# Performance work log

Hardware: AMD Instinct MI355X
Metric: run time of the kernel (lower is better)

## Reference

```python
import jax, jax.numpy as jnp
from jax import lax
import numpy as np

DIM = 128    # block channel dim C
RESO = 56    # H = W = patches_resolution
HEADS = 4    # block num_heads (each branch uses HEADS//2)
SPLIT = 2    # split_size (stripe width)
MLP_RATIO = 4
BATCH = 32


def _ln(x, g, b, eps=1e-5):
    mu = jnp.mean(x, axis=-1, keepdims=True)
    var = jnp.mean(jnp.square(x - mu), axis=-1, keepdims=True)
    return (x - mu) * lax.rsqrt(var + eps) * g + b


def _lepe_attn(q, k, v, cw, cb, H, W, H_sp, W_sp, heads):
    # q,k,v: (B, L=H*W, C). Cross-shaped window attention with depthwise-conv LePE.
    B, L, C = q.shape
    hd = C // heads
    scale = hd ** -0.5
    nH, nW = H // H_sp, W // W_sp
    tok = H_sp * W_sp

    def to_win(t):  # im2cswin: (B,L,C) -> (B*nH*nW, heads, tok, hd)
        t = t.transpose(0, 2, 1).reshape(B, C, H, W)
        t = t.reshape(B, C, nH, H_sp, nW, W_sp).transpose(0, 2, 4, 3, 5, 1)
        return t.reshape(-1, tok, heads, hd).transpose(0, 2, 1, 3)

    qw = to_win(q) * scale
    kw = to_win(k)

    # v as per-window images (B*nW_total, C, H_sp, W_sp) for the depthwise conv LePE
    vimg = v.transpose(0, 2, 1).reshape(B, C, H, W)
    vimg = vimg.reshape(B, C, nH, H_sp, nW, W_sp).transpose(0, 2, 4, 1, 3, 5).reshape(-1, C, H_sp, W_sp)
    lepe = lax.conv_general_dilated(vimg, cw, (1, 1), 'SAME', feature_group_count=C,
                                    dimension_numbers=('NCHW', 'OIHW', 'NCHW')) + cb[None, :, None, None]
    lepe = lepe.reshape(-1, heads, hd, tok).transpose(0, 1, 3, 2)  # (W', heads, tok, hd)
    vw = vimg.reshape(-1, heads, hd, tok).transpose(0, 1, 3, 2)

    attn = jax.nn.softmax(jnp.einsum('whqd,whkd->whqk', qw, kw), axis=-1)
    out = jnp.einsum('whqk,whkd->whqd', attn, vw) + lepe        # (W', heads, tok, hd)
    out = out.transpose(0, 2, 1, 3).reshape(-1, tok, C)
    # windows2img -> (B, H*W, C)
    out = out.reshape(B, nH, nW, H_sp, W_sp, C).transpose(0, 1, 3, 2, 4, 5).reshape(B, H * W, C)
    return out


def setup_inputs() -> dict:
    key = jax.random.key(0)
    ks = jax.random.split(key, 12)
    B, L, C = BATCH, RESO * RESO, DIM
    Ch = C // 2
    Hid = C * MLP_RATIO
    s = 0.02
    f32 = jnp.float32
    return {
        'x':       jax.random.normal(ks[0], (B, L, C), f32),
        'norm1_g': jnp.ones((C,), f32), 'norm1_b': jnp.zeros((C,), f32),
        'qkv_w':   jax.random.normal(ks[1], (C, 3 * C), f32) * s,
        'proj_w':  jax.random.normal(ks[2], (C, C), f32) * s,
        'proj_b':  jnp.zeros((C,), f32),
        'conv_w0': jax.random.normal(ks[3], (Ch, 1, 3, 3), f32) * s,
        'conv_b0': jnp.zeros((Ch,), f32),
        'conv_w1': jax.random.normal(ks[4], (Ch, 1, 3, 3), f32) * s,
        'conv_b1': jnp.zeros((Ch,), f32),
        'norm2_g': jnp.ones((C,), f32), 'norm2_b': jnp.zeros((C,), f32),
        'fc1_w':   jax.random.normal(ks[5], (C, Hid), f32) * s,
        'fc1_b':   jnp.zeros((Hid,), f32),
        'fc2_w':   jax.random.normal(ks[6], (Hid, C), f32) * s,
        'fc2_b':   jnp.zeros((C,), f32),
    }


def reference(x, norm1_g, norm1_b, qkv_w, proj_w, proj_b, conv_w0, conv_b0,
              conv_w1, conv_b1, norm2_g, norm2_b, fc1_w, fc1_b, fc2_w, fc2_b):
    B, L, C = x.shape
    H = W = RESO
    Ch = C // 2
    h = HEADS // 2

    img = _ln(x, norm1_g, norm1_b)
    qkv = (img @ qkv_w).reshape(B, L, 3, C)
    q, k, v = qkv[:, :, 0], qkv[:, :, 1], qkv[:, :, 2]

    # branch 0 (idx=0): H_sp = reso, W_sp = split  |  branch 1 (idx=1): H_sp = split, W_sp = reso
    x1 = _lepe_attn(q[..., :Ch], k[..., :Ch], v[..., :Ch], conv_w0, conv_b0, H, W, H, SPLIT, h)
    x2 = _lepe_attn(q[..., Ch:], k[..., Ch:], v[..., Ch:], conv_w1, conv_b1, H, W, SPLIT, W, h)

    att = jnp.concatenate([x1, x2], axis=2) @ proj_w + proj_b
    x = x + att
    y = _ln(x, norm2_g, norm2_b)
    y = jax.nn.gelu(y @ fc1_w + fc1_b, approximate=False) @ fc2_w + fc2_b
    return x + y
```

## Files before the change

### kernel.cpp

```cpp
#include <hip/hip_runtime.h>
#include <hip/hip_bf16.h>
#include <math.h>

#define NTOK 100352
typedef __attribute__((ext_vector_type(8))) short short8_t;
typedef __attribute__((ext_vector_type(4))) float f32x4;

union I4S8 { int4 i; short h[8]; short8_t v; };

__device__ __forceinline__ short f2bf(float f) {
    union { float f; unsigned u; } x; x.f = f;
    unsigned r = x.u + 0x7FFFu + ((x.u >> 16) & 1u);
    return (short)(r >> 16);
}
__device__ __forceinline__ float bf2f(short s) {
    union { unsigned u; float f; } x; x.u = ((unsigned)(unsigned short)s) << 16;
    return x.f;
}

__global__ void prep_weights(const float* __restrict__ qkv_w, const float* __restrict__ proj_w,
                             const float* __restrict__ fc1_w, const float* __restrict__ fc2_w,
                             short* __restrict__ wt) {
    int idx = blockIdx.x * 256 + threadIdx.x;
    const float* src; int K, N, base;
    if (idx < 49152)       { src = qkv_w;  K = 128; N = 384; base = 0; }
    else if (idx < 65536)  { src = proj_w; K = 128; N = 128; base = 49152; }
    else if (idx < 131072) { src = fc1_w;  K = 128; N = 512; base = 65536; }
    else                   { src = fc2_w;  K = 512; N = 128; base = 131072; }
    int local = idx - base;
    int n = local / K, k = local - n * K;
    wt[idx] = f2bf(src[k * N + n]);
}

__global__ __launch_bounds__(256) void ln_kernel(const float* __restrict__ in,
                                                 const float* __restrict__ g,
                                                 const float* __restrict__ b,
                                                 short* __restrict__ out) {
    int token = blockIdx.x * 4 + (threadIdx.x >> 6);
    int lane = threadIdx.x & 63;
    const float2 v = *reinterpret_cast<const float2*>(in + (size_t)token * 128 + lane * 2);
    float s = v.x + v.y;
    float sq = v.x * v.x + v.y * v.y;
    #pragma unroll
    for (int m = 32; m >= 1; m >>= 1) {
        s  += __shfl_xor(s, m);
        sq += __shfl_xor(sq, m);
    }
    float mean = s * (1.0f / 128.0f);
    float var = sq * (1.0f / 128.0f) - mean * mean;
    float rstd = rsqrtf(var + 1e-5f);
    float2 gg = *reinterpret_cast<const float2*>(g + lane * 2);
    float2 bb = *reinterpret_cast<const float2*>(b + lane * 2);
    float o0 = (v.x - mean) * rstd * gg.x + bb.x;
    float o1 = (v.y - mean) * rstd * gg.y + bb.y;
    unsigned pack = ((unsigned)(unsigned short)f2bf(o0)) |
                    (((unsigned)(unsigned short)f2bf(o1)) << 16);
    *reinterpret_cast<unsigned*>(out + (size_t)token * 128 + lane * 2) = pack;
}

template<int EPI>
__global__ __launch_bounds__(256) void gemm_kernel(const short* __restrict__ A,
                                                   const short* __restrict__ BT,
                                                   const float* __restrict__ bias,
                                                   const float* __restrict__ res,
                                                   void* __restrict__ out,
                                                   int N, int K) {
    __shared__ short As[64][136];
    __shared__ short Bs[64][136];
    const int m0 = blockIdx.x * 64;
    const int n0 = blockIdx.y * 64;
    const int tid = threadIdx.x;
    const int w = tid >> 6, lane = tid & 63;
    const int r = lane & 15, g = lane >> 4;

    f32x4 acc[4] = { {0.f,0.f,0.f,0.f}, {0.f,0.f,0.f,0.f},
                     {0.f,0.f,0.f,0.f}, {0.f,0.f,0.f,0.f} };

    for (int kc = 0; kc < K; kc += 128) {
        for (int i = tid; i < 1024; i += 256) {
            int row = i >> 4, seg = i & 15;
            int4 va = *reinterpret_cast<const int4*>(A + (size_t)(m0 + row) * K + kc + seg * 8);
            *reinterpret_cast<int4*>(&As[row][seg * 8]) = va;
            int4 vb = *reinterpret_cast<const int4*>(BT + (size_t)(n0 + row) * K + kc + seg * 8);
            *reinterpret_cast<int4*>(&Bs[row][seg * 8]) = vb;
        }
        __syncthreads();
        #pragma unroll
        for (int ks = 0; ks < 4; ++ks) {
            short8_t af = *reinterpret_cast<const short8_t*>(&As[w * 16 + r][ks * 32 + g * 8]);
            #pragma unroll
            for (int nt = 0; nt < 4; ++nt) {
                short8_t bfr = *reinterpret_cast<const short8_t*>(&Bs[nt * 16 + r][ks * 32 + g * 8]);
                acc[nt] = __builtin_amdgcn_mfma_f32_16x16x32_bf16(af, bfr, acc[nt], 0, 0, 0);
            }
        }
        __syncthreads();
    }

    #pragma unroll
    for (int nt = 0; nt < 4; ++nt) {
        int col = n0 + nt * 16 + r;
        float bv = (EPI != 0) ? bias[col] : 0.f;
        #pragma unroll
        for (int j = 0; j < 4; ++j) {
            int row = m0 + w * 16 + g * 4 + j;
            float v = acc[nt][j];
            if (EPI == 0) {
                ((short*)out)[(size_t)row * N + col] = f2bf(v);
            } else if (EPI == 1) {
                ((float*)out)[(size_t)row * N + col] = v + bv + res[(size_t)row * N + col];
            } else {
                float t = v + bv;
                float ge = 0.5f * t * (1.0f + erff(t * 0.70710678118654752f));
                ((short*)out)[(size_t)row * N + col] = f2bf(ge);
            }
        }
    }
}

__global__ __launch_bounds__(256) void attn_kernel(const short* __restrict__ qkv,
                                                   const float* __restrict__ cw0,
                                                   const float* __restrict__ cb0,
                                                   const float* __restrict__ cw1,
                                                   const float* __restrict__ cb1,
                                                   short* __restrict__ attout) {
    __shared__ short P[112][120];
    __shared__ short vT[32][120];

    const int win = blockIdx.x;
    const int head = blockIdx.y;
    const int type = blockIdx.z;
    const int b = win / 28;
    const int wdx = win - b * 28;
    const int tid = threadIdx.x;
    const int wv = tid >> 6, lane = tid & 63;
    const int r = lane & 15, g = lane >> 4;
    const int chb = type * 64 + head * 32;
    const float* cw = type ? cw1 : cw0;
    const float* cb = type ? cb1 : cb0;

    auto rowof = [&](int t) -> int {
        int l;
        if (type == 0) { int hs = t >> 1, wsp = t & 1; l = hs * 56 + wdx * 2 + wsp; }
        else           { int hs = (t >= 56) ? 1 : 0, wsp = t - hs * 56; l = (wdx * 2 + hs) * 56 + wsp; }
        return b * 3136 + l;
    };

    for (int i = tid; i < 448; i += 256) {
        int tt = i >> 2, seg = i & 3;
        int roww = rowof(tt);
        I4S8 u; u.i = *reinterpret_cast<const int4*>(qkv + (size_t)roww * 384 + 256 + chb + seg * 8);
        #pragma unroll
        for (int j = 0; j < 8; ++j) vT[seg * 8 + j][tt] = u.h[j];
    }

    short8_t kf[7];
    #pragma unroll
    for (int nt = 0; nt < 7; ++nt) {
        int roww = rowof(nt * 16 + r);
        kf[nt] = *reinterpret_cast<const short8_t*>(qkv + (size_t)roww * 384 + 128 + chb + g * 8);
    }

    f32x4 sa[2][7];
    #pragma unroll
    for (int t = 0; t < 2; ++t)
        #pragma unroll
        for (int nt = 0; nt < 7; ++nt)
            sa[t][nt] = (f32x4){0.f, 0.f, 0.f, 0.f};

    #pragma unroll
    for (int t = 0; t < 2; ++t) {
        int mt = wv + 4 * t;
        if (mt < 7) {
            int roww = rowof(mt * 16 + r);
            short8_t af = *reinterpret_cast<const short8_t*>(qkv + (size_t)roww * 384 + chb + g * 8);
            #pragma unroll
            for (int nt = 0; nt < 7; ++nt)
                sa[t][nt] = __builtin_amdgcn_mfma_f32_16x16x32_bf16(af, kf[nt], sa[t][nt], 0, 0, 0);
        }
    }

    const float scale = 0.17677669529663687f;
    #pragma unroll
    for (int t = 0; t < 2; ++t) {
        int mt = wv + 4 * t;
        if (mt < 7) {
            #pragma unroll
            for (int j = 0; j < 4; ++j) {
                float sv[7];
                float mx = -1e30f;
                #pragma unroll
                for (int nt = 0; nt < 7; ++nt) { sv[nt] = sa[t][nt][j] * scale; mx = fmaxf(mx, sv[nt]); }
                #pragma unroll
                for (int m = 8; m >= 1; m >>= 1) mx = fmaxf(mx, __shfl_xor(mx, m));
                float sum = 0.f;
                #pragma unroll
                for (int nt = 0; nt < 7; ++nt) { sv[nt] = __expf(sv[nt] - mx); sum += sv[nt]; }
                #pragma unroll
                for (int m = 8; m >= 1; m >>= 1) sum += __shfl_xor(sum, m);
                float inv = 1.0f / sum;
                int row = mt * 16 + g * 4 + j;
                #pragma unroll
                for (int nt = 0; nt < 7; ++nt)
                    P[row][nt * 16 + r] = f2bf(sv[nt] * inv);
            }
        }
    }
    __syncthreads();

    #pragma unroll
    for (int t = 0; t < 4; ++t) {
        int idx = wv + 4 * t;
        if (idx < 14) {
            int mt = idx >> 1, nt = idx & 1;
            int m0 = mt * 16, n0 = nt * 16;
            f32x4 acc = {0.f, 0.f, 0.f, 0.f};
            #pragma unroll
            for (int ks = 0; ks < 4; ++ks) {
                short8_t pa, vb;
                if (ks < 3 || g < 2) {
                    int k0 = ks * 32 + g * 8;
                    pa = *reinterpret_cast<const short8_t*>(&P[m0 + r][k0]);
                    vb = *reinterpret_cast<const short8_t*>(&vT[n0 + r][k0]);
                } else {
                    #pragma unroll
                    for (int j = 0; j < 8; ++j) { pa[j] = 0; vb[j] = 0; }
                }
                acc = __builtin_amdgcn_mfma_f32_16x16x32_bf16(pa, vb, acc, 0, 0, 0);
            }
            int d = n0 + r;
            int cl = head * 32 + d;
            float w9[9];
            #pragma unroll
            for (int j = 0; j < 9; ++j) w9[j] = cw[cl * 9 + j];
            float cbias = cb[cl];
            #pragma unroll
            for (int j = 0; j < 4; ++j) {
                int tok = m0 + g * 4 + j;
                float v = acc[j];
                int hs, wsp;
                if (type == 0) { hs = tok >> 1; wsp = tok & 1; }
                else           { hs = (tok >= 56) ? 1 : 0; wsp = tok - hs * 56; }
                float lp = cbias;
                #pragma unroll
                for (int ky = 0; ky < 3; ++ky) {
                    int hh = hs + ky - 1;
                    bool okh = (type == 0) ? (hh >= 0 && hh < 56) : (hh >= 0 && hh < 2);
                    #pragma unroll
                    for (int kx = 0; kx < 3; ++kx) {
                        int wwp = wsp + kx - 1;
                        bool okw = (type == 0) ? (wwp >= 0 && wwp < 2) : (wwp >= 0 && wwp < 56);
                        if (okh && okw) {
                            int tt = (type == 0) ? (hh * 2 + wwp) : (hh * 56 + wwp);
                            lp += w9[ky * 3 + kx] * bf2f(vT[d][tt]);
                        }
                    }
                }
                v += lp;
                int roww = rowof(tok);
                attout[(size_t)roww * 128 + chb + d] = f2bf(v);
            }
        }
    }
}

extern "C" void kernel_launch(void* const* d_in, const int* in_sizes, int n_in,
                              void* d_out, int out_size, void* d_ws, size_t ws_size,
                              hipStream_t stream) {
    const float* x      = (const float*)d_in[0];
    const float* n1g    = (const float*)d_in[1];
    const float* n1b    = (const float*)d_in[2];
    const float* qkv_w  = (const float*)d_in[3];
    const float* proj_w = (const float*)d_in[4];
    const float* proj_b = (const float*)d_in[5];
    const float* cw0    = (const float*)d_in[6];
    const float* cb0    = (const float*)d_in[7];
    const float* cw1    = (const float*)d_in[8];
    const float* cb1    = (const float*)d_in[9];
    const float* n2g    = (const float*)d_in[10];
    const float* n2b    = (const float*)d_in[11];
    const float* fc1_w  = (const float*)d_in[12];
    const float* fc1_b  = (const float*)d_in[13];
    const float* fc2_w  = (const float*)d_in[14];
    const float* fc2_b  = (const float*)d_in[15];
    float* out = (float*)d_out;
    char* ws = (char*)d_ws;

    short* img   = (short*)(ws + 0);
    short* qkv   = (short*)(ws + 25690112);
    short* att   = (short*)(ws + 102760448);
    float* xres  = (float*)(ws + 128450560);
    short* wT    = (short*)(ws + 179830784);
    short* wqkvT  = wT;
    short* wprojT = wT + 49152;
    short* wfc1T  = wT + 65536;
    short* wfc2T  = wT + 131072;
    short* hidden = qkv;
    short* y2     = img;

    prep_weights<<<768, 256, 0, stream>>>(qkv_w, proj_w, fc1_w, fc2_w, wT);
    ln_kernel<<<25088, 256, 0, stream>>>(x, n1g, n1b, img);
    gemm_kernel<0><<<dim3(1568, 6), 256, 0, stream>>>(img, wqkvT, nullptr, nullptr, qkv, 384, 128);
    attn_kernel<<<dim3(896, 2, 2), 256, 0, stream>>>(qkv, cw0, cb0, cw1, cb1, att);
    gemm_kernel<1><<<dim3(1568, 2), 256, 0, stream>>>(att, wprojT, proj_b, x, xres, 128, 128);
    ln_kernel<<<25088, 256, 0, stream>>>(xres, n2g, n2b, y2);
    gemm_kernel<2><<<dim3(1568, 8), 256, 0, stream>>>(y2, wfc1T, fc1_b, nullptr, hidden, 512, 128);
    gemm_kernel<1><<<dim3(1568, 2), 256, 0, stream>>>(hidden, wfc2T, fc2_b, xres, out, 128, 512);
}
```

Before: 383.6 us.

## Use 128x128 GEMM tiles with direct global-to-LDS A loads and register B fragments

The GEMM kernel moves from 64x64 tiles to 128x128 tiles arranged as 2x2 waves, each computing a 64x64 sub-tile. A tiles are loaded straight from global memory into LDS with an XOR swizzle to avoid bank conflicts. B fragments are read from global memory directly into registers instead of being staged in shared memory. This cuts global re-reads of A and weights and raises MFMA work per load, at the cost of more accumulator registers (64 floats per thread), possibly lower occupancy, and uncoalesced B fragment loads.

```diff
diff --git a/kernel.cpp b/kernel.cpp
--- a/kernel.cpp
+++ b/kernel.cpp
@@ -17,6 +17,10 @@
     union { unsigned u; float f; } x; x.u = ((unsigned)(unsigned short)s) << 16;
     return x.f;
 }
+
+#define GLDS16(gsrc, ldst) __builtin_amdgcn_global_load_lds( \
+    (const __attribute__((address_space(1))) unsigned int*)(gsrc), \
+    (__attribute__((address_space(3))) unsigned int*)(ldst), 16, 0, 0)
 
 __global__ void prep_weights(const float* __restrict__ qkv_w, const float* __restrict__ proj_w,
                              const float* __restrict__ fc1_w, const float* __restrict__ fc2_w,
@@ -65,54 +69,75 @@
                                                    const float* __restrict__ res,
                                                    void* __restrict__ out,
                                                    int N, int K) {
-    __shared__ short As[64][136];
-    __shared__ short Bs[64][136];
-    const int m0 = blockIdx.x * 64;
-    const int n0 = blockIdx.y * 64;
+    __shared__ short As[128 * 64];
+    const int m0 = blockIdx.x * 128;
+    const int n0 = blockIdx.y * 128;
     const int tid = threadIdx.x;
     const int w = tid >> 6, lane = tid & 63;
+    const int wr = w >> 1, wc = w & 1;
     const int r = lane & 15, g = lane >> 4;
 
-    f32x4 acc[4] = { {0.f,0.f,0.f,0.f}, {0.f,0.f,0.f,0.f},
-                     {0.f,0.f,0.f,0.f}, {0.f,0.f,0.f,0.f} };
-
-    for (int kc = 0; kc < K; kc += 128) {
-        for (int i = tid; i < 1024; i += 256) {
-            int row = i >> 4, seg = i & 15;
-            int4 va = *reinterpret_cast<const int4*>(A + (size_t)(m0 + row) * K + kc + seg * 8);
-            *reinterpret_cast<int4*>(&As[row][seg * 8]) = va;
-            int4 vb = *reinterpret_cast<const int4*>(BT + (size_t)(n0 + row) * K + kc + seg * 8);
-            *reinterpret_cast<int4*>(&Bs[row][seg * 8]) = vb;
-        }
+    f32x4 acc[4][4];
+    #pragma unroll
+    for (int i = 0; i < 4; ++i)
+        #pragma unroll
+        for (int j = 0; j < 4; ++j) acc[i][j] = (f32x4){0.f, 0.f, 0.f, 0.f};
+
+    const int srow_in_issue = lane >> 3;
+    const int sseg_lane = lane & 7;
+
+    for (int kc = 0; kc < K; kc += 64) {
+        #pragma unroll
+        for (int t = 0; t < 4; ++t) {
+            int row = w * 32 + t * 8 + srow_in_issue;
+            int sseg = sseg_lane ^ (row & 7);
+            const short* gsrc = A + (size_t)(m0 + row) * K + kc + sseg * 8;
+            GLDS16(gsrc, &As[(w * 32 + t * 8) * 64]);
+        }
+        short8_t bfr[2][4];
+        #pragma unroll
+        for (int ks = 0; ks < 2; ++ks)
+            #pragma unroll
+            for (int nf = 0; nf < 4; ++nf) {
+                int brow = n0 + wc * 64 + nf * 16 + r;
+                bfr[ks][nf] = *reinterpret_cast<const short8_t*>(
+                    BT + (size_t)brow * K + kc + ks * 32 + g * 8);
+            }
         __syncthreads();
         #pragma unroll
-        for (int ks = 0; ks < 4; ++ks) {
-            short8_t af = *reinterpret_cast<const short8_t*>(&As[w * 16 + r][ks * 32 + g * 8]);
-            #pragma unroll
-            for (int nt = 0; nt < 4; ++nt) {
-                short8_t bfr = *reinterpret_cast<const short8_t*>(&Bs[nt * 16 + r][ks * 32 + g * 8]);
-                acc[nt] = __builtin_amdgcn_mfma_f32_16x16x32_bf16(af, bfr, acc[nt], 0, 0, 0);
+        for (int ks = 0; ks < 2; ++ks) {
+            #pragma unroll
+            for (int mf = 0; mf < 4; ++mf) {
+                int arow = wr * 64 + mf * 16 + r;
+                int s0 = (ks * 4 + g) ^ (arow & 7);
+                short8_t af = *reinterpret_cast<const short8_t*>(&As[arow * 64 + s0 * 8]);
+                #pragma unroll
+                for (int nf = 0; nf < 4; ++nf)
+                    acc[mf][nf] = __builtin_amdgcn_mfma_f32_16x16x32_bf16(af, bfr[ks][nf], acc[mf][nf], 0, 0, 0);
             }
         }
         __syncthreads();
     }
 
     #pragma unroll
-    for (int nt = 0; nt < 4; ++nt) {
-        int col = n0 + nt * 16 + r;
+    for (int nf = 0; nf < 4; ++nf) {
+        int col = n0 + wc * 64 + nf * 16 + r;
         float bv = (EPI != 0) ? bias[col] : 0.f;
         #pragma unroll
-        for (int j = 0; j < 4; ++j) {
-            int row = m0 + w * 16 + g * 4 + j;
-            float v = acc[nt][j];
-            if (EPI == 0) {
-                ((short*)out)[(size_t)row * N + col] = f2bf(v);
-            } else if (EPI == 1) {
-                ((float*)out)[(size_t)row * N + col] = v + bv + res[(size_t)row * N + col];
-            } else {
-                float t = v + bv;
-                float ge = 0.5f * t * (1.0f + erff(t * 0.70710678118654752f));
-                ((short*)out)[(size_t)row * N + col] = f2bf(ge);
+        for (int mf = 0; mf < 4; ++mf) {
+            #pragma unroll
+            for (int j = 0; j < 4; ++j) {
+                int row = m0 + wr * 64 + mf * 16 + g * 4 + j;
+                float v = acc[mf][nf][j];
+                if (EPI == 0) {
+                    ((short*)out)[(size_t)row * N + col] = f2bf(v);
+                } else if (EPI == 1) {
+                    ((float*)out)[(size_t)row * N + col] = v + bv + res[(size_t)row * N + col];
+                } else {
+                    float t = v + bv;
+                    float ge = 0.5f * t * (1.0f + erff(t * 0.70710678118654752f));
+                    ((short*)out)[(size_t)row * N + col] = f2bf(ge);
+                }
             }
         }
     }
@@ -300,10 +325,10 @@
 
     prep_weights<<<768, 256, 0, stream>>>(qkv_w, proj_w, fc1_w, fc2_w, wT);
     ln_kernel<<<25088, 256, 0, stream>>>(x, n1g, n1b, img);
-    gemm_kernel<0><<<dim3(1568, 6), 256, 0, stream>>>(img, wqkvT, nullptr, nullptr, qkv, 384, 128);
+    gemm_kernel<0><<<dim3(784, 3), 256, 0, stream>>>(img, wqkvT, nullptr, nullptr, qkv, 384, 128);
     attn_kernel<<<dim3(896, 2, 2), 256, 0, stream>>>(qkv, cw0, cb0, cw1, cb1, att);
-    gemm_kernel<1><<<dim3(1568, 2), 256, 0, stream>>>(att, wprojT, proj_b, x, xres, 128, 128);
+    gemm_kernel<1><<<dim3(784, 1), 256, 0, stream>>>(att, wprojT, proj_b, x, xres, 128, 128);
     ln_kernel<<<25088, 256, 0, stream>>>(xres, n2g, n2b, y2);
-    gemm_kernel<2><<<dim3(1568, 8), 256, 0, stream>>>(y2, wfc1T, fc1_b, nullptr, hidden, 512, 128);
-    gemm_kernel<1><<<dim3(1568, 2), 256, 0, stream>>>(hidden, wfc2T, fc2_b, xres, out, 128, 512);
-}
+    gemm_kernel<2><<<dim3(784, 4), 256, 0, stream>>>(y2, wfc1T, fc1_b, nullptr, hidden, 512, 128);
+    gemm_kernel<1><<<dim3(784, 1), 256, 0, stream>>>(hidden, wfc2T, fc2_b, xres, out, 128, 512);
+}
```

After: 401.1 us. 1.05x slower.

## Fuse MLP fc1+GELU+fc2 via LDS and use register-resident weight GEMMs

Applied to the files above, without the earlier changes.

Replaces the LDS-staged GEMM with a kernel that keeps the 64-column weight slice in registers and streams A fragments directly from global memory, with several M tiles per block and vectorised packed stores. Fuses fc1, GELU and fc2 into one kernel that holds the 512-wide hidden activation per 64-row tile in swizzled shared memory, so the large hidden tensor never goes to HBM. Replaces erff with a polynomial erf approximation (Abramowitz-Stegun) for GELU. The risks are slightly less accurate GELU, and register pressure and occupancy limits from the launch bounds.

```diff
diff --git a/kernel.cpp b/kernel.cpp
--- a/kernel.cpp
+++ b/kernel.cpp
@@ -16,6 +16,19 @@
 __device__ __forceinline__ float bf2f(short s) {
     union { unsigned u; float f; } x; x.u = ((unsigned)(unsigned short)s) << 16;
     return x.f;
+}
+__device__ __forceinline__ unsigned pk2(float a, float b) {
+    return ((unsigned)(unsigned short)f2bf(a)) | (((unsigned)(unsigned short)f2bf(b)) << 16);
+}
+__device__ __forceinline__ float gelu(float x) {
+    float z = x * 0.70710678118654752f;
+    float az = fabsf(z);
+    float t = 1.0f / (1.0f + 0.3275911f * az);
+    float poly = t * (0.254829592f + t * (-0.284496736f + t * (1.421413741f +
+                 t * (-1.453152027f + t * 1.061405429f))));
+    float e = 1.0f - poly * __expf(-az * az);
+    float erfv = (z < 0.f) ? -e : e;
+    return 0.5f * x * (1.0f + erfv);
 }
 
 __global__ void prep_weights(const float* __restrict__ qkv_w, const float* __restrict__ proj_w,
@@ -58,62 +71,160 @@
     *reinterpret_cast<unsigned*>(out + (size_t)token * 128 + lane * 2) = pack;
 }
 
-template<int EPI>
-__global__ __launch_bounds__(256) void gemm_kernel(const short* __restrict__ A,
-                                                   const short* __restrict__ BT,
-                                                   const float* __restrict__ bias,
-                                                   const float* __restrict__ res,
-                                                   void* __restrict__ out,
-                                                   int N, int K) {
-    __shared__ short As[64][136];
-    __shared__ short Bs[64][136];
-    const int m0 = blockIdx.x * 64;
-    const int n0 = blockIdx.y * 64;
+template<int EPI, int IT>
+__global__ __launch_bounds__(256, 4) void sgemm(const short* __restrict__ A,
+                                                const short* __restrict__ WT,
+                                                const float* __restrict__ bias,
+                                                const float* __restrict__ resid,
+                                                short* __restrict__ outb,
+                                                float* __restrict__ outf,
+                                                int N) {
     const int tid = threadIdx.x;
     const int w = tid >> 6, lane = tid & 63;
     const int r = lane & 15, g = lane >> 4;
-
-    f32x4 acc[4] = { {0.f,0.f,0.f,0.f}, {0.f,0.f,0.f,0.f},
-                     {0.f,0.f,0.f,0.f}, {0.f,0.f,0.f,0.f} };
-
-    for (int kc = 0; kc < K; kc += 128) {
-        for (int i = tid; i < 1024; i += 256) {
-            int row = i >> 4, seg = i & 15;
-            int4 va = *reinterpret_cast<const int4*>(A + (size_t)(m0 + row) * K + kc + seg * 8);
-            *reinterpret_cast<int4*>(&As[row][seg * 8]) = va;
-            int4 vb = *reinterpret_cast<const int4*>(BT + (size_t)(n0 + row) * K + kc + seg * 8);
-            *reinterpret_cast<int4*>(&Bs[row][seg * 8]) = vb;
+    const int c0 = blockIdx.y * 64;
+    const int m0 = blockIdx.x * (64 * IT);
+
+    short8_t bfr[4][4];
+    #pragma unroll
+    for (int nt = 0; nt < 4; ++nt)
+        #pragma unroll
+        for (int kf = 0; kf < 4; ++kf)
+            bfr[nt][kf] = *reinterpret_cast<const short8_t*>(
+                WT + (size_t)(c0 + nt * 16 + r) * 128 + kf * 32 + g * 8);
+
+    #pragma unroll 2
+    for (int it = 0; it < IT; ++it) {
+        const int mrow = m0 + (it * 4 + w) * 16;
+        short8_t af[4];
+        #pragma unroll
+        for (int kf = 0; kf < 4; ++kf)
+            af[kf] = *reinterpret_cast<const short8_t*>(
+                A + (size_t)(mrow + r) * 128 + kf * 32 + g * 8);
+        f32x4 acc[4];
+        #pragma unroll
+        for (int nt = 0; nt < 4; ++nt) acc[nt] = (f32x4){0.f, 0.f, 0.f, 0.f};
+        #pragma unroll
+        for (int kf = 0; kf < 4; ++kf)
+            #pragma unroll
+            for (int nt = 0; nt < 4; ++nt)
+                acc[nt] = __builtin_amdgcn_mfma_f32_16x16x32_bf16(bfr[nt][kf], af[kf], acc[nt], 0, 0, 0);
+
+        const int row = mrow + r;
+        if (EPI == 0) {
+            #pragma unroll
+            for (int nt = 0; nt < 4; ++nt) {
+                int col = c0 + nt * 16 + g * 4;
+                uint2 p;
+                p.x = pk2(acc[nt][0], acc[nt][1]);
+                p.y = pk2(acc[nt][2], acc[nt][3]);
+                *reinterpret_cast<uint2*>(&outb[(size_t)row * N + col]) = p;
+            }
+        } else {
+            #pragma unroll
+            for (int nt = 0; nt < 4; ++nt) {
+                int col = c0 + nt * 16 + g * 4;
+                f32x4 b4 = *reinterpret_cast<const f32x4*>(&bias[col]);
+                f32x4 x4 = *reinterpret_cast<const f32x4*>(&resid[(size_t)row * 128 + col]);
+                f32x4 v;
+                #pragma unroll
+                for (int j = 0; j < 4; ++j) v[j] = acc[nt][j] + b4[j] + x4[j];
+                *reinterpret_cast<f32x4*>(&outf[(size_t)row * 128 + col]) = v;
+            }
+        }
+    }
+}
+
+__global__ __launch_bounds__(256, 4) void mlp_kernel(const short* __restrict__ Y,
+                                                     const short* __restrict__ W1T,
+                                                     const float* __restrict__ b1,
+                                                     const short* __restrict__ W2T,
+                                                     const float* __restrict__ b2,
+                                                     const float* __restrict__ xres,
+                                                     float* __restrict__ out) {
+    __shared__ short hid[64 * 256];
+    const int m0 = blockIdx.x * 64;
+    const int tid = threadIdx.x;
+    const int w = tid >> 6, lane = tid & 63;
+    const int r = lane & 15, g = lane >> 4;
+
+    f32x4 acc2[4][2];
+    #pragma unroll
+    for (int tt = 0; tt < 4; ++tt)
+        #pragma unroll
+        for (int o = 0; o < 2; ++o) acc2[tt][o] = (f32x4){0.f, 0.f, 0.f, 0.f};
+
+    #pragma unroll
+    for (int c = 0; c < 2; ++c) {
+        #pragma unroll
+        for (int mf = 0; mf < 4; ++mf) {
+            f32x4 acc[4];
+            #pragma unroll
+            for (int nt = 0; nt < 4; ++nt) acc[nt] = (f32x4){0.f, 0.f, 0.f, 0.f};
+            #pragma unroll
+            for (int kf = 0; kf < 4; ++kf) {
+                short8_t afk = *reinterpret_cast<const short8_t*>(
+                    Y + (size_t)(m0 + mf * 16 + r) * 128 + kf * 32 + g * 8);
+                #pragma unroll
+                for (int nt = 0; nt < 4; ++nt) {
+                    short8_t bf1 = *reinterpret_cast<const short8_t*>(
+                        W1T + (size_t)(c * 256 + w * 64 + nt * 16 + r) * 128 + kf * 32 + g * 8);
+                    acc[nt] = __builtin_amdgcn_mfma_f32_16x16x32_bf16(bf1, afk, acc[nt], 0, 0, 0);
+                }
+            }
+            int row = mf * 16 + r;
+            #pragma unroll
+            for (int nt = 0; nt < 4; ++nt) {
+                int lc = w * 64 + nt * 16 + g * 4;
+                int col = c * 256 + lc;
+                f32x4 b4 = *reinterpret_cast<const f32x4*>(&b1[col]);
+                float h0 = gelu(acc[nt][0] + b4[0]);
+                float h1 = gelu(acc[nt][1] + b4[1]);
+                float h2 = gelu(acc[nt][2] + b4[2]);
+                float h3 = gelu(acc[nt][3] + b4[3]);
+                int seg = lc >> 3;
+                int half = (lc >> 2) & 1;
+                int sw = (seg & 24) | ((seg ^ row) & 7);
+                uint2 p; p.x = pk2(h0, h1); p.y = pk2(h2, h3);
+                *reinterpret_cast<uint2*>((char*)hid + row * 512 + sw * 16 + half * 8) = p;
+            }
         }
         __syncthreads();
         #pragma unroll
-        for (int ks = 0; ks < 4; ++ks) {
-            short8_t af = *reinterpret_cast<const short8_t*>(&As[w * 16 + r][ks * 32 + g * 8]);
-            #pragma unroll
-            for (int nt = 0; nt < 4; ++nt) {
-                short8_t bfr = *reinterpret_cast<const short8_t*>(&Bs[nt * 16 + r][ks * 32 + g * 8]);
-                acc[nt] = __builtin_amdgcn_mfma_f32_16x16x32_bf16(af, bfr, acc[nt], 0, 0, 0);
-            }
+        for (int kq = 0; kq < 8; ++kq) {
+            short8_t bf2[2], hf[4];
+            #pragma unroll
+            for (int o = 0; o < 2; ++o)
+                bf2[o] = *reinterpret_cast<const short8_t*>(
+                    W2T + (size_t)(w * 32 + o * 16 + r) * 512 + c * 256 + kq * 32 + g * 8);
+            #pragma unroll
+            for (int tt = 0; tt < 4; ++tt) {
+                int row = tt * 16 + r;
+                int seg = kq * 4 + g;
+                int sw = (seg & 24) | ((seg ^ row) & 7);
+                hf[tt] = *reinterpret_cast<const short8_t*>((char*)hid + row * 512 + sw * 16);
+            }
+            #pragma unroll
+            for (int tt = 0; tt < 4; ++tt)
+                #pragma unroll
+                for (int o = 0; o < 2; ++o)
+                    acc2[tt][o] = __builtin_amdgcn_mfma_f32_16x16x32_bf16(bf2[o], hf[tt], acc2[tt][o], 0, 0, 0);
         }
         __syncthreads();
     }
 
     #pragma unroll
-    for (int nt = 0; nt < 4; ++nt) {
-        int col = n0 + nt * 16 + r;
-        float bv = (EPI != 0) ? bias[col] : 0.f;
-        #pragma unroll
-        for (int j = 0; j < 4; ++j) {
-            int row = m0 + w * 16 + g * 4 + j;
-            float v = acc[nt][j];
-            if (EPI == 0) {
-                ((short*)out)[(size_t)row * N + col] = f2bf(v);
-            } else if (EPI == 1) {
-                ((float*)out)[(size_t)row * N + col] = v + bv + res[(size_t)row * N + col];
-            } else {
-                float t = v + bv;
-                float ge = 0.5f * t * (1.0f + erff(t * 0.70710678118654752f));
-                ((short*)out)[(size_t)row * N + col] = f2bf(ge);
-            }
+    for (int tt = 0; tt < 4; ++tt) {
+        int row = m0 + tt * 16 + r;
+        #pragma unroll
+        for (int o = 0; o < 2; ++o) {
+            int col = w * 32 + o * 16 + g * 4;
+            f32x4 b4 = *reinterpret_cast<const f32x4*>(&b2[col]);
+            f32x4 x4 = *reinterpret_cast<const f32x4*>(&xres[(size_t)row * 128 + col]);
+            f32x4 v;
+            #pragma unroll
+            for (int j = 0; j < 4; ++j) v[j] = acc2[tt][o][j] + b4[j] + x4[j];
+            *reinterpret_cast<f32x4*>(&out[(size_t)row * 128 + col]) = v;
         }
     }
 }
@@ -295,15 +406,13 @@
     short* wprojT = wT + 49152;
     short* wfc1T  = wT + 65536;
     short* wfc2T  = wT + 131072;
-    short* hidden = qkv;
     short* y2     = img;
 
     prep_weights<<<768, 256, 0, stream>>>(qkv_w, proj_w, fc1_w, fc2_w, wT);
     ln_kernel<<<25088, 256, 0, stream>>>(x, n1g, n1b, img);
-    gemm_kernel<0><<<dim3(1568, 6), 256, 0, stream>>>(img, wqkvT, nullptr, nullptr, qkv, 384, 128);
+    sgemm<0, 8><<<dim3(196, 6), 256, 0, stream>>>(img, wqkvT, nullptr, nullptr, qkv, nullptr, 384);
     attn_kernel<<<dim3(896, 2, 2), 256, 0, stream>>>(qkv, cw0, cb0, cw1, cb1, att);
-    gemm_kernel<1><<<dim3(1568, 2), 256, 0, stream>>>(att, wprojT, proj_b, x, xres, 128, 128);
+    sgemm<1, 4><<<dim3(392, 2), 256, 0, stream>>>(att, wprojT, proj_b, x, nullptr, xres, 128);
     ln_kernel<<<25088, 256, 0, stream>>>(xres, n2g, n2b, y2);
-    gemm_kernel<2><<<dim3(1568, 8), 256, 0, stream>>>(y2, wfc1T, fc1_b, nullptr, hidden, 512, 128);
-    gemm_kernel<1><<<dim3(1568, 2), 256, 0, stream>>>(hidden, wfc2T, fc2_b, xres, out, 128, 512);
-}
+    mlp_kernel<<<1568, 256, 0, stream>>>(y2, wfc1T, fc1_b, wfc2T, fc2_b, xres, out);
+}
```

Measured after the change: 461.9 us. 20.4% more time.
